# Performance work log

Hardware: AMD Instinct MI355X
Metric: run time of the kernel (lower is better)

The kernel has to match this reference:

```python
import jax, jax.numpy as jnp
import numpy as np

N_HEAD = 16
N_EMBD = 2048


def _rope(x):
    # x: (B, H, L, D). FAITHFUL to source: _apply_rope unpacks (B, L, H, D) on a
    # (B, H, L, D) tensor, so rotation angle = head_index * inv_freq, broadcast over
    # all sequence positions (a latent bug in the original, reproduced exactly).
    B, H, L, D = x.shape
    inv_freq = 1.0 / (10000.0 ** (jnp.arange(0, D, 2, dtype=jnp.float32) / D))  # (D/2,)
    theta = jnp.arange(H, dtype=jnp.float32)[:, None] * inv_freq[None, :]       # (H, D/2)
    cos = jnp.cos(theta)[None, :, None, :]  # (1, H, 1, D/2)
    sin = jnp.sin(theta)[None, :, None, :]
    xp = x.astype(jnp.float32).reshape(B, H, L, D // 2, 2)
    x0, x1 = xp[..., 0], xp[..., 1]
    r0 = x0 * cos - x1 * sin
    r1 = x0 * sin + x1 * cos
    return jnp.stack([r0, r1], axis=-1).reshape(B, H, L, D).astype(x.dtype)


def setup_inputs() -> dict:
    key = jax.random.key(0)
    k1, k2, k3 = jax.random.split(key, 3)
    B, L, C = 2, 2048, N_EMBD
    s = 1.0 / np.sqrt(C).astype(np.float32)
    x = jax.random.normal(k1, (B, L, C), dtype=jnp.float32)
    w_attn = jax.random.normal(k2, (3 * C, C), dtype=jnp.float32) * s
    w_proj = jax.random.normal(k3, (C, C), dtype=jnp.float32) * s
    return {"x": x, "w_attn": w_attn, "w_proj": w_proj}


def reference(x, w_attn, w_proj):
    B, L, C = x.shape
    H = N_HEAD
    D = C // H
    qkv = x @ w_attn.T                       # (B, L, 3C)
    q, k, v = jnp.split(qkv, 3, axis=2)
    q = q.reshape(B, L, H, D).transpose(0, 2, 1, 3)  # (B, H, L, D)
    k = k.reshape(B, L, H, D).transpose(0, 2, 1, 3)
    v = v.reshape(B, L, H, D).transpose(0, 2, 1, 3)
    q = _rope(q)
    k = _rope(k)
    attn = jnp.einsum('bhqd,bhkd->bhqk', q, k) * (1.0 / np.sqrt(D).astype(np.float32))
    causal = jnp.tril(jnp.ones((L, L), dtype=bool))
    attn = jnp.where(causal[None, None], attn, -jnp.inf)
    attn = jax.nn.softmax(attn, axis=-1)
    y = jnp.einsum('bhqk,bhkd->bhqd', attn, v)
    y = y.transpose(0, 2, 1, 3).reshape(B, L, C)
    return y @ w_proj.T
```

## Files before the change

### kernel.cpp

```cpp
#include <hip/hip_runtime.h>

typedef __attribute__((ext_vector_type(8))) short bf16x8;
typedef __attribute__((ext_vector_type(4))) float f32x4;

__device__ __forceinline__ unsigned short f2bf(float f) {
  unsigned int u = __float_as_uint(f);
  u += 0x7FFF + ((u >> 16) & 1);
  return (unsigned short)(u >> 16);
}

__device__ __forceinline__ void gload_lds16(const void* g, void* l) {
  __builtin_amdgcn_global_load_lds(
      (const __attribute__((address_space(1))) unsigned int*)g,
      (__attribute__((address_space(3))) unsigned int*)l,
      16, 0, 0);
}

__global__ void cast_f32_to_bf16(const float* __restrict__ in,
                                 unsigned short* __restrict__ out, int n4) {
  int stride = gridDim.x * blockDim.x;
  for (int i = blockIdx.x * blockDim.x + threadIdx.x; i < n4; i += stride) {
    float4 v = ((const float4*)in)[i];
    ushort4 o;
    o.x = f2bf(v.x); o.y = f2bf(v.y); o.z = f2bf(v.z); o.w = f2bf(v.w);
    ((ushort4*)out)[i] = o;
  }
}

template<int EPI>
__global__ __launch_bounds__(256, 4)
void gemm_bt(const unsigned short* __restrict__ A,
             const unsigned short* __restrict__ Bw,
             float* __restrict__ Cf,
             unsigned short* __restrict__ Qo,
             unsigned short* __restrict__ Ko,
             unsigned short* __restrict__ Vo,
             int M, int N, int K, int Lseq, int nbx) {
  __shared__ unsigned short As[2][128 * 32];
  __shared__ unsigned short Bs[2][128 * 32];
  const int tid = threadIdx.x;
  const int lane = tid & 63, w = tid >> 6;
  const int wm = w >> 1, wn = w & 1;
  const int g4 = lane >> 4, r16 = lane & 15;

  const int nwg = gridDim.x;
  const int cpx = nwg >> 3;
  const int bid = (blockIdx.x & 7) * cpx + (blockIdx.x >> 3);
  const long arow0 = (long)(bid / nbx) * 128;
  const long brow0 = (long)(bid % nbx) * 128;

#define STAGE_G(k0_, buf_)                                                    \
  do {                                                                        \
    _Pragma("unroll")                                                         \
    for (int c_ = 0; c_ < 2; ++c_) {                                          \
      int off_ = (w << 11) + (c_ << 10) + (lane << 4);                        \
      int row_ = off_ >> 6;                                                   \
      int cbs_ = ((off_ >> 4) & 3) ^ ((row_ >> 1) & 3);                       \
      gload_lds16(A + (arow0 + row_) * (long)K + (k0_) + cbs_ * 8,            \
                  (char*)As[buf_] + off_);                                    \
      gload_lds16(Bw + (brow0 + row_) * (long)K + (k0_) + cbs_ * 8,           \
                  (char*)Bs[buf_] + off_);                                    \
    }                                                                         \
  } while (0)

  f32x4 acc[4][4];
#pragma unroll
  for (int i = 0; i < 4; ++i)
#pragma unroll
    for (int j = 0; j < 4; ++j) acc[i][j] = (f32x4){0.f, 0.f, 0.f, 0.f};

  const int T = K >> 5;
  int cur = 0;
  STAGE_G(0, 0);

  for (int t = 0; t < T; ++t) {
    if (t < T - 1) {
      STAGE_G((t + 1) << 5, cur ^ 1);
      asm volatile("s_waitcnt vmcnt(4)" ::: "memory");
    } else {
      asm volatile("s_waitcnt vmcnt(0)" ::: "memory");
    }
    __builtin_amdgcn_s_barrier();

    const int rb = g4 ^ ((r16 >> 1) & 3);
    bf16x8 af[4], bf[4];
#pragma unroll
    for (int mf = 0; mf < 4; ++mf)
      af[mf] = *(const bf16x8*)((const char*)As[cur] +
                                ((64 * wm + 16 * mf + r16) << 6) + (rb << 4));
#pragma unroll
    for (int nf = 0; nf < 4; ++nf)
      bf[nf] = *(const bf16x8*)((const char*)Bs[cur] +
                                ((64 * wn + 16 * nf + r16) << 6) + (rb << 4));
#pragma unroll
    for (int mf = 0; mf < 4; ++mf)
#pragma unroll
      for (int nf = 0; nf < 4; ++nf)
        acc[mf][nf] = __builtin_amdgcn_mfma_f32_16x16x32_bf16(
            af[mf], bf[nf], acc[mf][nf], 0, 0, 0);
    asm volatile("" ::: "memory");
    __builtin_amdgcn_s_barrier();
    cur ^= 1;
  }
#undef STAGE_G

  const float qscale = 0.08838834764831845f;
#pragma unroll
  for (int mf = 0; mf < 4; ++mf) {
#pragma unroll
    for (int nf = 0; nf < 4; ++nf) {
#pragma unroll
      for (int i = 0; i < 4; ++i) {
        long row = arow0 + 64 * wm + 16 * mf + 4 * g4 + i;
        long col = brow0 + 64 * wn + 16 * nf + r16;
        float v = acc[mf][nf][i];
        if (EPI == 0) {
          Cf[row * N + col] = v;
        } else {
          int which = (int)(col >> 11);
          int h = ((int)col >> 7) & 15;
          int d = (int)col & 127;
          int b = (int)(row >> 11);
          int l = (int)row & 2047;
          long bhead = (long)(b * 16 + h);
          if (which == 0)
            Qo[(bhead * Lseq + l) * 128 + d] = f2bf(v * qscale);
          else if (which == 1)
            Ko[(bhead * Lseq + l) * 128 + d] = f2bf(v);
          else
            Vo[(bhead * 128 + d) * Lseq + l] = f2bf(v);
        }
      }
    }
  }
}

__global__ __launch_bounds__(256, 2)
void attn_fwd(const unsigned short* __restrict__ Q,
              const unsigned short* __restrict__ K,
              const unsigned short* __restrict__ Vt,
              unsigned short* __restrict__ Y, int L) {
  const int D = 128;
  const int id = blockIdx.x;
  const int g = id & 7, kk = id >> 3;
  const int bh = (g << 2) + (kk >> 5);
  const int qt = 31 - (kk & 31);
  const int tid = threadIdx.x, lane = tid & 63, w = tid >> 6;
  const int g4 = lane >> 4, r16 = lane & 15;
  const int q0 = qt * 64;

  __shared__ unsigned short Klds[2 * 64 * 128];
  __shared__ unsigned short Vlds[2 * 128 * 64];
  __shared__ unsigned short P[4][16][72];

  const unsigned short* Qh = Q + (long)bh * L * D;
  const unsigned short* Kh = K + (long)bh * L * D;
  const unsigned short* Vh = Vt + (long)bh * D * L;

#define STAGE_TILE(kt_, buf_)                                                 \
  do {                                                                        \
    const int kbase_ = (kt_) * 64;                                            \
    _Pragma("unroll")                                                         \
    for (int r_ = 0; r_ < 4; ++r_) {                                          \
      int off_ = (tid << 4) + (r_ << 12);                                     \
      int krow_ = off_ >> 8, kcb_ = (off_ >> 4) & 15;                         \
      int kcbs_ = kcb_ ^ (krow_ & 7);                                         \
      gload_lds16(Kh + (long)(kbase_ + krow_) * 128 + kcbs_ * 8,              \
                  (char*)Klds + (buf_)*16384 + (w << 10) + (r_ << 12));       \
      int vrow_ = off_ >> 7, vcb_ = (off_ >> 4) & 7;                          \
      int vcbs_ = vcb_ ^ (vrow_ & 7);                                         \
      gload_lds16(Vh + (long)vrow_ * L + kbase_ + vcbs_ * 8,                  \
                  (char*)Vlds + (buf_)*16384 + (w << 10) + (r_ << 12));       \
    }                                                                         \
  } while (0)

  bf16x8 qf[4];
  {
    long qrow = q0 + 16 * w + r16;
#pragma unroll
    for (int ks = 0; ks < 4; ++ks)
      qf[ks] = *(const bf16x8*)(Qh + qrow * D + ks * 32 + g4 * 8);
  }
  f32x4 o[8];
#pragma unroll
  for (int j = 0; j < 8; ++j) o[j] = (f32x4){0.f, 0.f, 0.f, 0.f};
  float mrun[4] = {-1e30f, -1e30f, -1e30f, -1e30f};
  float lrun[4] = {0.f, 0.f, 0.f, 0.f};

  int cur = 0;
  STAGE_TILE(0, 0);

  for (int kt = 0; kt <= qt; ++kt) {
    if (kt < qt) {
      STAGE_TILE(kt + 1, cur ^ 1);
      asm volatile("s_waitcnt vmcnt(8)" ::: "memory");
    } else {
      asm volatile("s_waitcnt vmcnt(0)" ::: "memory");
    }
    __builtin_amdgcn_s_barrier();

    const char* Kl = (const char*)Klds + cur * 16384;
    const char* Vl = (const char*)Vlds + cur * 16384;

    f32x4 s[4];
#pragma unroll
    for (int nf = 0; nf < 4; ++nf) s[nf] = (f32x4){0.f, 0.f, 0.f, 0.f};
#pragma unroll
    for (int ks = 0; ks < 4; ++ks) {
#pragma unroll
      for (int nf = 0; nf < 4; ++nf) {
        int row = 16 * nf + r16;
        bf16x8 kf = *(const bf16x8*)(Kl + row * 256 +
                                     (((ks * 4 + g4) ^ (row & 7)) << 4));
        s[nf] = __builtin_amdgcn_mfma_f32_16x16x32_bf16(qf[ks], kf, s[nf], 0, 0, 0);
      }
    }

    const bool diag = (kt == qt);
#pragma unroll
    for (int i = 0; i < 4; ++i) {
      int qg = q0 + 16 * w + 4 * g4 + i;
      float sv[4];
      float rmax = -1e30f;
#pragma unroll
      for (int nf = 0; nf < 4; ++nf) {
        float t = s[nf][i];
        if (diag && (kt * 64 + 16 * nf + r16) > qg) t = -1e30f;
        sv[nf] = t;
        rmax = fmaxf(rmax, t);
      }
      rmax = fmaxf(rmax, __shfl_xor(rmax, 1));
      rmax = fmaxf(rmax, __shfl_xor(rmax, 2));
      rmax = fmaxf(rmax, __shfl_xor(rmax, 4));
      rmax = fmaxf(rmax, __shfl_xor(rmax, 8));
      float mnew = fmaxf(mrun[i], rmax);
      float corr = __expf(mrun[i] - mnew);
      mrun[i] = mnew;
      float rs = 0.f;
#pragma unroll
      for (int nf = 0; nf < 4; ++nf) {
        float pv = __expf(sv[nf] - mnew);
        P[w][4 * g4 + i][16 * nf + r16] = f2bf(pv);
        rs += pv;
      }
      rs += __shfl_xor(rs, 1);
      rs += __shfl_xor(rs, 2);
      rs += __shfl_xor(rs, 4);
      rs += __shfl_xor(rs, 8);
      lrun[i] = lrun[i] * corr + rs;
#pragma unroll
      for (int nf2 = 0; nf2 < 8; ++nf2) o[nf2][i] *= corr;
    }
#pragma unroll
    for (int ks2 = 0; ks2 < 2; ++ks2) {
      bf16x8 pf = *(const bf16x8*)(&P[w][r16][ks2 * 32 + g4 * 8]);
#pragma unroll
      for (int nf2 = 0; nf2 < 8; ++nf2) {
        int row = 16 * nf2 + r16;
        bf16x8 vf = *(const bf16x8*)(Vl + row * 128 +
                                     (((ks2 * 4 + g4) ^ (row & 7)) << 4));
        o[nf2] = __builtin_amdgcn_mfma_f32_16x16x32_bf16(pf, vf, o[nf2], 0, 0, 0);
      }
    }
    asm volatile("" ::: "memory");
    __builtin_amdgcn_s_barrier();
    cur ^= 1;
  }
#undef STAGE_TILE

  const int b = bh >> 4, h = bh & 15;
#pragma unroll
  for (int nf2 = 0; nf2 < 8; ++nf2) {
#pragma unroll
    for (int i = 0; i < 4; ++i) {
      long row = (long)b * L + q0 + 16 * w + 4 * g4 + i;
      float v = o[nf2][i] / lrun[i];
      Y[row * 2048 + h * 128 + 16 * nf2 + r16] = f2bf(v);
    }
  }
}

extern "C" void kernel_launch(void* const* d_in, const int* in_sizes, int n_in,
                              void* d_out, int out_size, void* d_ws,
                              size_t ws_size, hipStream_t stream) {
  const float* x = (const float*)d_in[0];
  const float* wa = (const float*)d_in[1];
  const float* wp = (const float*)d_in[2];
  float* out = (float*)d_out;
  const int B = 2, L = 2048, C = 2048;
  const int M = B * L;

  unsigned short* xb = (unsigned short*)d_ws;
  unsigned short* wab = xb + (size_t)M * C;
  unsigned short* wpb = wab + (size_t)3 * C * C;
  unsigned short* Qb = wpb + (size_t)C * C;
  unsigned short* Kb = Qb + (size_t)M * C;
  unsigned short* Vb = Kb + (size_t)M * C;
  unsigned short* Yb = Vb + (size_t)M * C;

  cast_f32_to_bf16<<<2048, 256, 0, stream>>>(x, xb, M * C / 4);
  cast_f32_to_bf16<<<2048, 256, 0, stream>>>(wa, wab, 3 * C * C / 4);
  cast_f32_to_bf16<<<1024, 256, 0, stream>>>(wp, wpb, C * C / 4);

  gemm_bt<1><<<(M / 128) * (3 * C / 128), 256, 0, stream>>>(
      xb, wab, nullptr, Qb, Kb, Vb, M, 3 * C, C, L, 3 * C / 128);

  attn_fwd<<<1024, 256, 0, stream>>>(Qb, Kb, Vb, Yb, L);

  gemm_bt<0><<<(M / 128) * (C / 128), 256, 0, stream>>>(
      Yb, wpb, out, nullptr, nullptr, nullptr, M, C, C, L, C / 128);
}
```

Baseline: 345.7 us.

## Add 256x256-tile 8-wave pipelined GEMM for QKV projection

Introduces a new GEMM kernel with 256x256 block tiles, 512 threads (8 waves), 64-wide K steps and double-buffered direct-to-LDS loads. Loads are interleaved across eight phases with s_setprio around the MFMA bursts. It is used only for the QKV projection. The aim is more operand reuse per LDS byte and better overlap of global loads with MFMA work. The cost is higher register pressure (128 accumulator floats per thread) and only 384 blocks, which may not fill all CUs evenly.

```diff
diff --git a/kernel.cpp b/kernel.cpp
--- a/kernel.cpp
+++ b/kernel.cpp
@@ -15,6 +15,9 @@
       (__attribute__((address_space(3))) unsigned int*)l,
       16, 0, 0);
 }
+
+#define MF(a, b, c) __builtin_amdgcn_mfma_f32_16x16x32_bf16((a), (b), (c), 0, 0, 0)
+#define FENCE asm volatile("" ::: "memory")
 
 __global__ void cast_f32_to_bf16(const float* __restrict__ in,
                                  unsigned short* __restrict__ out, int n4) {
@@ -25,6 +28,156 @@
     o.x = f2bf(v.x); o.y = f2bf(v.y); o.z = f2bf(v.z); o.w = f2bf(v.w);
     ((ushort4*)out)[i] = o;
   }
+}
+
+template<int EPI>
+__global__ __launch_bounds__(512, 2)
+void gemm8p(const unsigned short* __restrict__ A,
+            const unsigned short* __restrict__ Bw,
+            float* __restrict__ Cf,
+            unsigned short* __restrict__ Qo,
+            unsigned short* __restrict__ Ko,
+            unsigned short* __restrict__ Vo,
+            int M, int N, int K, int Lseq) {
+  __shared__ unsigned short lds[2][2][2][8192];
+  const int tid = threadIdx.x;
+  const int lane = tid & 63, w = tid >> 6;
+  const int wm = w >> 2, wn = w & 3;
+  const int bh = wn >> 1;
+  const int bcol = (wn & 1) * 64;
+  const int g4 = lane >> 4, r16 = lane & 15;
+  const long arow0 = (long)blockIdx.y * 256;
+  const long brow0 = (long)blockIdx.x * 256;
+
+#define LDA(db, mf, kk)                                                       \
+  (*(const bf16x8*)((const char*)&lds[0][db][wm][0] +                         \
+                    (((mf)*16 + r16) << 7) +                                  \
+                    ((((kk)*4 + g4) ^ (r16 & 7)) << 4)))
+#define LDB(db, nf, kk)                                                       \
+  (*(const bf16x8*)((const char*)&lds[1][db][bh][0] +                         \
+                    ((bcol + (nf)*16 + r16) << 7) +                           \
+                    ((((kk)*4 + g4) ^ (r16 & 7)) << 4)))
+
+#define STG(mat, db, half, kt)                                                \
+  do {                                                                        \
+    const unsigned short* g_ = (mat) ? Bw : A;                                \
+    long r0_ = ((mat) ? brow0 : arow0) + (half)*128;                          \
+    int k0_ = (kt) << 6;                                                      \
+    _Pragma("unroll")                                                         \
+    for (int c_ = 0; c_ < 2; ++c_) {                                          \
+      int off_ = (c_ << 13) + (tid << 4);                                     \
+      int row_ = off_ >> 7;                                                   \
+      int scb_ = ((off_ >> 4) & 7) ^ (row_ & 7);                              \
+      gload_lds16(g_ + (r0_ + row_) * (long)K + k0_ + scb_ * 8,               \
+                  (char*)&lds[mat][db][half][0] + off_);                      \
+    }                                                                         \
+  } while (0)
+
+  f32x4 acc[8][4];
+#pragma unroll
+  for (int i = 0; i < 8; ++i)
+#pragma unroll
+    for (int j = 0; j < 4; ++j) acc[i][j] = (f32x4){0.f, 0.f, 0.f, 0.f};
+
+  bf16x8 b00, b01, b10, b11, b20, b21, b30, b31;
+
+#define PH(db, q, STAGE_STMT, VMSTMT)                                         \
+  do {                                                                        \
+    bf16x8 a00 = LDA(db, 2*(q), 0), a01 = LDA(db, 2*(q), 1);                  \
+    bf16x8 a10 = LDA(db, 2*(q)+1, 0), a11 = LDA(db, 2*(q)+1, 1);              \
+    STAGE_STMT;                                                               \
+    VMSTMT;                                                                   \
+    FENCE; __builtin_amdgcn_s_barrier(); FENCE;                               \
+    __builtin_amdgcn_s_setprio(1);                                            \
+    acc[2*(q)][0] = MF(a00, b00, acc[2*(q)][0]);                              \
+    acc[2*(q)][0] = MF(a01, b01, acc[2*(q)][0]);                              \
+    acc[2*(q)][1] = MF(a00, b10, acc[2*(q)][1]);                              \
+    acc[2*(q)][1] = MF(a01, b11, acc[2*(q)][1]);                              \
+    acc[2*(q)][2] = MF(a00, b20, acc[2*(q)][2]);                              \
+    acc[2*(q)][2] = MF(a01, b21, acc[2*(q)][2]);                              \
+    acc[2*(q)][3] = MF(a00, b30, acc[2*(q)][3]);                              \
+    acc[2*(q)][3] = MF(a01, b31, acc[2*(q)][3]);                              \
+    acc[2*(q)+1][0] = MF(a10, b00, acc[2*(q)+1][0]);                          \
+    acc[2*(q)+1][0] = MF(a11, b01, acc[2*(q)+1][0]);                          \
+    acc[2*(q)+1][1] = MF(a10, b10, acc[2*(q)+1][1]);                          \
+    acc[2*(q)+1][1] = MF(a11, b11, acc[2*(q)+1][1]);                          \
+    acc[2*(q)+1][2] = MF(a10, b20, acc[2*(q)+1][2]);                          \
+    acc[2*(q)+1][2] = MF(a11, b21, acc[2*(q)+1][2]);                          \
+    acc[2*(q)+1][3] = MF(a10, b30, acc[2*(q)+1][3]);                          \
+    acc[2*(q)+1][3] = MF(a11, b31, acc[2*(q)+1][3]);                          \
+    __builtin_amdgcn_s_setprio(0);                                            \
+    FENCE; __builtin_amdgcn_s_barrier(); FENCE;                               \
+  } while (0)
+
+#define LOADB(db)                                                             \
+  do {                                                                        \
+    b00 = LDB(db, 0, 0); b01 = LDB(db, 0, 1);                                 \
+    b10 = LDB(db, 1, 0); b11 = LDB(db, 1, 1);                                 \
+    b20 = LDB(db, 2, 0); b21 = LDB(db, 2, 1);                                 \
+    b30 = LDB(db, 3, 0); b31 = LDB(db, 3, 1);                                 \
+  } while (0)
+
+#define VM4 asm volatile("s_waitcnt vmcnt(4)" ::: "memory")
+
+  const int NT = K >> 6;
+  STG(0, 0, 0, 0); STG(0, 0, 1, 0);
+  STG(1, 0, 0, 0); STG(1, 0, 1, 0);
+  STG(1, 1, 0, 1); STG(1, 1, 1, 1);
+  VM4;
+  FENCE; __builtin_amdgcn_s_barrier(); FENCE;
+
+  for (int i = 0; i < (NT >> 1); ++i) {
+    const int t1 = 2 * i + 1;
+    int n0 = 2 * i + 2; if (n0 > NT - 1) n0 = NT - 1;
+    int n1 = 2 * i + 3; if (n1 > NT - 1) n1 = NT - 1;
+    LOADB(0);
+    PH(0, 0, STG(0, 1, 0, t1), );
+    PH(0, 1, STG(0, 1, 1, t1), );
+    PH(0, 2, STG(1, 0, 0, n0), );
+    PH(0, 3, STG(1, 0, 1, n0), VM4);
+    LOADB(1);
+    PH(1, 0, STG(0, 0, 0, n0), );
+    PH(1, 1, STG(0, 0, 1, n0), );
+    PH(1, 2, STG(1, 1, 0, n1), );
+    PH(1, 3, STG(1, 1, 1, n1), VM4);
+  }
+  asm volatile("s_waitcnt vmcnt(0)" ::: "memory");
+
+  const float qscale = 0.08838834764831845f;
+#pragma unroll
+  for (int mf = 0; mf < 8; ++mf) {
+#pragma unroll
+    for (int nf = 0; nf < 4; ++nf) {
+#pragma unroll
+      for (int i = 0; i < 4; ++i) {
+        long row = arow0 + wm * 128 + mf * 16 + 4 * g4 + i;
+        long col = brow0 + wn * 64 + nf * 16 + r16;
+        float v = acc[mf][nf][i];
+        if (EPI == 0) {
+          Cf[row * N + col] = v;
+        } else {
+          int which = (int)(col >> 11);
+          int h = ((int)col >> 7) & 15;
+          int d = (int)col & 127;
+          int b = (int)(row >> 11);
+          int l = (int)row & 2047;
+          long bhead = (long)(b * 16 + h);
+          if (which == 0)
+            Qo[(bhead * Lseq + l) * 128 + d] = f2bf(v * qscale);
+          else if (which == 1)
+            Ko[(bhead * Lseq + l) * 128 + d] = f2bf(v);
+          else
+            Vo[(bhead * 128 + d) * Lseq + l] = f2bf(v);
+        }
+      }
+    }
+  }
+#undef LDA
+#undef LDB
+#undef STG
+#undef PH
+#undef LOADB
+#undef VM4
 }
 
 template<int EPI>
@@ -96,8 +249,7 @@
     for (int mf = 0; mf < 4; ++mf)
 #pragma unroll
       for (int nf = 0; nf < 4; ++nf)
-        acc[mf][nf] = __builtin_amdgcn_mfma_f32_16x16x32_bf16(
-            af[mf], bf[nf], acc[mf][nf], 0, 0, 0);
+        acc[mf][nf] = MF(af[mf], bf[nf], acc[mf][nf]);
     asm volatile("" ::: "memory");
     __builtin_amdgcn_s_barrier();
     cur ^= 1;
@@ -212,7 +364,7 @@
         int row = 16 * nf + r16;
         bf16x8 kf = *(const bf16x8*)(Kl + row * 256 +
                                      (((ks * 4 + g4) ^ (row & 7)) << 4));
-        s[nf] = __builtin_amdgcn_mfma_f32_16x16x32_bf16(qf[ks], kf, s[nf], 0, 0, 0);
+        s[nf] = MF(qf[ks], kf, s[nf]);
       }
     }
 
@@ -259,7 +411,7 @@
         int row = 16 * nf2 + r16;
         bf16x8 vf = *(const bf16x8*)(Vl + row * 128 +
                                      (((ks2 * 4 + g4) ^ (row & 7)) << 4));
-        o[nf2] = __builtin_amdgcn_mfma_f32_16x16x32_bf16(pf, vf, o[nf2], 0, 0, 0);
+        o[nf2] = MF(pf, vf, o[nf2]);
       }
     }
     asm volatile("" ::: "memory");
@@ -302,8 +454,8 @@
   cast_f32_to_bf16<<<2048, 256, 0, stream>>>(wa, wab, 3 * C * C / 4);
   cast_f32_to_bf16<<<1024, 256, 0, stream>>>(wp, wpb, C * C / 4);
 
-  gemm_bt<1><<<(M / 128) * (3 * C / 128), 256, 0, stream>>>(
-      xb, wab, nullptr, Qb, Kb, Vb, M, 3 * C, C, L, 3 * C / 128);
+  gemm8p<1><<<dim3(3 * C / 256, M / 256), 512, 0, stream>>>(
+      xb, wab, nullptr, Qb, Kb, Vb, M, 3 * C, C, L);
 
   attn_fwd<<<1024, 256, 0, stream>>>(Qb, Kb, Vb, Yb, L);
 
```

Result: faster. 332.8 us (-3.7%).
